# Performance work log

Measured on AMD Instinct MI355X. Metric: run time of the kernel, lower is better.

## Reference

```python
import jax, jax.numpy as jnp
import numpy as np

V, C, H, L, BLK = 32000, 1024, 16, 4, 1024
B, T = 4, 1024
FF = 100
HD = C // H
EPS = 1e-5


def setup_inputs() -> dict:
    key = jax.random.key(0)
    ks = jax.random.split(key, 16)
    n = lambda k, s: (jax.random.normal(k, s, dtype=jnp.float32) * 0.02)
    inp = {
        "idx": jax.random.randint(ks[0], (B, T), 0, V),
        "tok_emb": n(ks[1], (V, C)),
        "pos_emb": n(ks[2], (BLK, C)),
        "Wq": n(ks[3], (L, C, C)), "bq": jnp.zeros((L, C)),
        "Wk": n(ks[4], (L, C, C)), "bk": jnp.zeros((L, C)),
        "Wv": n(ks[5], (L, C, C)), "bv": jnp.zeros((L, C)),
        "Wo": n(ks[6], (L, C, C)), "bo": jnp.zeros((L, C)),
        "ln1_w": jnp.ones((L, C)), "ln1_b": jnp.zeros((L, C)),
        "ln2_w": jnp.ones((L, C)), "ln2_b": jnp.zeros((L, C)),
        "W1": n(ks[7], (L, C, FF)), "b1": jnp.zeros((L, FF)),
        "W2": n(ks[8], (L, FF, C)), "b2": jnp.zeros((L, C)),
        "lnf_w": jnp.ones((C,)), "lnf_b": jnp.zeros((C,)),
    }
    return inp


def _ln(x, w, b):
    m = jnp.mean(x, -1, keepdims=True)
    v = jnp.mean(jnp.square(x - m), -1, keepdims=True)
    return (x - m) * jax.lax.rsqrt(v + EPS) * w + b


def reference(idx, tok_emb, pos_emb, Wq, bq, Wk, bk, Wv, bv, Wo, bo,
              ln1_w, ln1_b, ln2_w, ln2_b, W1, b1, W2, b2, lnf_w, lnf_b):
    Bn, Tn = idx.shape
    x = tok_emb[idx] + pos_emb[:Tn][None]  # [B,T,C]; dropout is identity at eval
    scale = 1.0 / np.sqrt(HD).astype(np.float32)
    att_maps = []
    for l in range(L):
        h = _ln(x, ln1_w[l], ln1_b[l])
        q = (h @ Wq[l] + bq[l]).reshape(Bn, Tn, H, HD).transpose(0, 2, 1, 3)
        k = (h @ Wk[l] + bk[l]).reshape(Bn, Tn, H, HD).transpose(0, 2, 1, 3)
        v = (h @ Wv[l] + bv[l]).reshape(Bn, Tn, H, HD).transpose(0, 2, 1, 3)
        att = jax.nn.softmax(jnp.einsum("bhqd,bhkd->bhqk", q, k) * scale, axis=-1)
        y = jnp.einsum("bhqk,bhkd->bhqd", att, v).transpose(0, 2, 1, 3).reshape(Bn, Tn, C)
        x = x + (y @ Wo[l] + bo[l])
        f = _ln(x, ln2_w[l], ln2_b[l])
        f = jax.nn.relu(f @ W1[l] + b1[l]) @ W2[l] + b2[l]
        x = x + f
        att_maps.append(att.mean(0))  # [H,T,T]
    x = _ln(x, lnf_w, lnf_b)
    pooled = x.mean(1)  # [B,C]
    return pooled, jnp.stack(att_maps)  # [L,H,T,T]
```

## Files before the change

### kernel.cpp

```cpp
#include <hip/hip_runtime.h>

typedef __bf16 bf16;
typedef __bf16 bf16x4 __attribute__((ext_vector_type(4)));
typedef __bf16 bf16x8 __attribute__((ext_vector_type(8)));
typedef float  f32x4  __attribute__((ext_vector_type(4)));

static constexpr int kC   = 1024;
static constexpr int kT   = 1024;
static constexpr int kB   = 4;
static constexpr int kH   = 16;
static constexpr int kHD  = 64;
static constexpr int kL   = 4;
static constexpr int kFF  = 100;
static constexpr int kFFP = 128;
static constexpr int kM   = kB * kT;

__device__ __forceinline__ void gload16(const bf16* g, bf16* l)
{
    __builtin_amdgcn_global_load_lds(
        (const __attribute__((address_space(1))) void*)g,
        (__attribute__((address_space(3))) void*)l, 16, 0, 0);
}

__device__ __forceinline__ unsigned bpack(float a, float b)
{
    bf16 x = (bf16)a, y = (bf16)b;
    unsigned short ux = __builtin_bit_cast(unsigned short, x);
    unsigned short uy = __builtin_bit_cast(unsigned short, y);
    return (unsigned)ux | ((unsigned)uy << 16);
}
__device__ __forceinline__ float blo(unsigned u) { return __builtin_bit_cast(float, u << 16); }
__device__ __forceinline__ float bhi(unsigned u) { return __builtin_bit_cast(float, u & 0xffff0000u); }

__global__ __launch_bounds__(256)
void prep_kernel(const float* __restrict__ Wq, const float* __restrict__ Wk,
                 const float* __restrict__ Wv, const float* __restrict__ Wo,
                 const float* __restrict__ W1, const float* __restrict__ W2,
                 const float* __restrict__ bq, const float* __restrict__ bk,
                 const float* __restrict__ bv,
                 bf16* __restrict__ WQKVT, bf16* __restrict__ WOT,
                 bf16* __restrict__ W1T, bf16* __restrict__ W2T,
                 float* __restrict__ BQKV, float* __restrict__ pooled)
{
    __shared__ float tile[32][33];
    const int bid = blockIdx.x, tid = threadIdx.x;
    const float* src; bf16* dst; int K, N, KP, NP, bx, by;
    if (bid < 12288) {
        const int slab = bid >> 10, within = bid & 1023;
        const int l = slab / 3, which = slab % 3;
        const float* W = (which == 0) ? Wq : (which == 1) ? Wk : Wv;
        src = W + (long)l * kC * kC;
        dst = WQKVT + (long)l * 3 * kC * kC + (long)which * kC * kC;
        K = N = KP = NP = kC; bx = within & 31; by = within >> 5;
    } else if (bid < 16384) {
        const int t = bid - 12288, z = t >> 10, within = t & 1023;
        src = Wo + (long)z * kC * kC; dst = WOT + (long)z * kC * kC;
        K = N = KP = NP = kC; bx = within & 31; by = within >> 5;
    } else if (bid < 16896) {
        const int t = bid - 16384, z = t >> 7, within = t & 127;
        src = W1 + (long)z * kC * kFF; dst = W1T + (long)z * kFFP * kC;
        K = kC; N = kFF; KP = kC; NP = kFFP; bx = within & 3; by = within >> 2;
    } else if (bid < 17408) {
        const int t = bid - 16896, z = t >> 7, within = t & 127;
        src = W2 + (long)z * kFF * kC; dst = W2T + (long)z * kC * kFFP;
        K = kFF; N = kC; KP = kFFP; NP = kC; bx = within & 31; by = within >> 5;
    } else if (bid < 17456) {
        const int gid = (bid - 17408) * 256 + tid;
        const int l = gid / (3 * kC), wq = (gid / kC) % 3, c = gid & (kC - 1);
        const float* s = (wq == 0) ? bq : (wq == 1) ? bk : bv;
        BQKV[gid] = s[l * kC + c];
        return;
    } else {
        const int i = (bid - 17456) * 256 + tid;
        if (i < kB * kC) pooled[i] = 0.f;
        return;
    }
    const int n0 = bx * 32, k0 = by * 32;
    const int tx = tid & 31, ty = tid >> 5;
#pragma unroll
    for (int i = 0; i < 4; ++i) {
        int k = k0 + ty + i * 8, n = n0 + tx;
        tile[ty + i * 8][tx] = (k < K && n < N) ? src[(long)k * N + n] : 0.f;
    }
    __syncthreads();
#pragma unroll
    for (int i = 0; i < 4; ++i) {
        int n = n0 + ty + i * 8, k = k0 + tx;
        if (n < NP && k < KP) dst[(long)n * KP + k] = (bf16)tile[tx][ty + i * 8];
    }
}

__global__ __launch_bounds__(256)
void embed_kernel(const int* __restrict__ idx, const float* __restrict__ tok,
                  const float* __restrict__ pos, float* __restrict__ x)
{
    const int m = blockIdx.x;
    const int c = threadIdx.x * 4;
    const int t = m & (kT - 1);
    const long tk = (long)idx[m] * kC;
    float4 a = *(const float4*)&tok[tk + c];
    float4 b = *(const float4*)&pos[(long)t * kC + c];
    float4 o; o.x = a.x + b.x; o.y = a.y + b.y; o.z = a.z + b.z; o.w = a.w + b.w;
    *(float4*)&x[(long)m * kC + c] = o;
}

__global__ __launch_bounds__(256)
void ln_kernel(const float* __restrict__ x, const float* __restrict__ g,
               const float* __restrict__ be, bf16* __restrict__ ob)
{
    __shared__ float red[8];
    const long row = blockIdx.x;
    const int tid = threadIdx.x, lane = tid & 63, wv = tid >> 6;
    const float4 v = *(const float4*)&x[row * kC + tid * 4];
    float s = v.x + v.y + v.z + v.w;
    float s2 = v.x * v.x + v.y * v.y + v.z * v.z + v.w * v.w;
#pragma unroll
    for (int o = 32; o > 0; o >>= 1) { s += __shfl_down(s, o); s2 += __shfl_down(s2, o); }
    if (!lane) { red[wv] = s; red[4 + wv] = s2; }
    __syncthreads();
    s  = red[0] + red[1] + red[2] + red[3];
    s2 = red[4] + red[5] + red[6] + red[7];
    const float mean = s * (1.f / kC);
    const float var  = s2 * (1.f / kC) - mean * mean;
    const float rstd = rsqrtf(var + 1e-5f);
    const float4 gg = *(const float4*)&g[tid * 4];
    const float4 bb = *(const float4*)&be[tid * 4];
    bf16x4 o;
    o[0] = (bf16)((v.x - mean) * rstd * gg.x + bb.x);
    o[1] = (bf16)((v.y - mean) * rstd * gg.y + bb.y);
    o[2] = (bf16)((v.z - mean) * rstd * gg.z + bb.z);
    o[3] = (bf16)((v.w - mean) * rstd * gg.w + bb.w);
    *(bf16x4*)&ob[row * kC + tid * 4] = o;
}

template<int WAVES_M, int WAVES_N, int AI, int BJ, int MODE, int GL>
__global__ __launch_bounds__(256)
void gemm_bf16(const bf16* __restrict__ Ag, long strideA,
               const bf16* __restrict__ Bg, long strideB,
               const float* __restrict__ bias, int strideBias,
               bf16* __restrict__ outb, long strideOut,
               float* __restrict__ resid,
               int N, int K, int lda, int ldb)
{
    constexpr int BM = WAVES_M * AI * 16;
    constexpr int BN = WAVES_N * BJ * 16;
    constexpr int BK = 64;
    constexpr int LK = GL ? BK : (BK + 8);
    __shared__ __align__(16) bf16 As[BM * LK];
    __shared__ __align__(16) bf16 Bs[BN * LK];
    const int tid = threadIdx.x, lane = tid & 63, wv = tid >> 6;
    const int wm = wv / WAVES_N, wn = wv % WAVES_N;
    const int lr = lane & 15, lg = lane >> 4;
    const int z = blockIdx.z;
    const bf16* A = Ag + (long)z * strideA;
    const bf16* B = Bg + (long)z * strideB;
    const float* bi = bias ? bias + (long)z * strideBias : nullptr;
    const int m0 = blockIdx.y * BM, n0 = blockIdx.x * BN;

    f32x4 acc[AI][BJ];
#pragma unroll
    for (int i = 0; i < AI; ++i)
#pragma unroll
        for (int j = 0; j < BJ; ++j) acc[i][j] = (f32x4){0.f, 0.f, 0.f, 0.f};

    for (int k0 = 0; k0 < K; k0 += BK) {
        if constexpr (GL) {
            static_assert((BM % 32) == 0 && (BN % 32) == 0, "GL tile multiple of 32");
            const int sr  = lane >> 3;
            const int gcb = (lane & 7) ^ sr;
            constexpr int ARW = BM / 4;
            constexpr int BRW = BN / 4;
#pragma unroll
            for (int p = 0; p < BM / 32; ++p)
                gload16(A + (long)(m0 + wv * ARW + p * 8 + sr) * lda + k0 + gcb * 8,
                        &As[(wv * ARW + p * 8) * BK]);
#pragma unroll
            for (int p = 0; p < BN / 32; ++p)
                gload16(B + (long)(n0 + wv * BRW + p * 8 + sr) * ldb + k0 + gcb * 8,
                        &Bs[(wv * BRW + p * 8) * BK]);
        } else {
            constexpr int AP = (BM * BK) / (256 * 8);
#pragma unroll
            for (int p = 0; p < AP; ++p) {
                int r = p * 32 + (tid >> 3), c = (tid & 7) * 8;
                *(uint4*)&As[r * LK + c] = *(const uint4*)&A[(long)(m0 + r) * lda + k0 + c];
            }
            constexpr int BP = (BN * BK) / (256 * 8);
#pragma unroll
            for (int p = 0; p < BP; ++p) {
                int r = p * 32 + (tid >> 3), c = (tid & 7) * 8;
                *(uint4*)&Bs[r * LK + c] = *(const uint4*)&B[(long)(n0 + r) * ldb + k0 + c];
            }
        }
        __syncthreads();
#pragma unroll
        for (int kk = 0; kk < 2; ++kk) {
            bf16x8 af[AI], bfv[BJ];
#pragma unroll
            for (int i = 0; i < AI; ++i) {
                const int r = wm * AI * 16 + i * 16 + lr;
                const int c = GL ? (((kk * 4 + lg) ^ (lr & 7)) * 8) : (kk * 32 + lg * 8);
                af[i] = *(const bf16x8*)&As[r * LK + c];
            }
#pragma unroll
            for (int j = 0; j < BJ; ++j) {
                const int r = wn * BJ * 16 + j * 16 + lr;
                const int c = GL ? (((kk * 4 + lg) ^ (lr & 7)) * 8) : (kk * 32 + lg * 8);
                bfv[j] = *(const bf16x8*)&Bs[r * LK + c];
            }
#pragma unroll
            for (int i = 0; i < AI; ++i)
#pragma unroll
                for (int j = 0; j < BJ; ++j)
                    acc[i][j] = __builtin_amdgcn_mfma_f32_16x16x32_bf16(af[i], bfv[j], acc[i][j], 0, 0, 0);
        }
        __syncthreads();
    }

#pragma unroll
    for (int i = 0; i < AI; ++i)
#pragma unroll
        for (int j = 0; j < BJ; ++j)
#pragma unroll
            for (int rr = 0; rr < 4; ++rr) {
                const int grow = m0 + wm * AI * 16 + i * 16 + lg * 4 + rr;
                const int gcol = n0 + wn * BJ * 16 + j * 16 + lr;
                float v = acc[i][j][rr];
                if constexpr (MODE == 0) {
                    v += bi[gcol];
                    if (z == 0) v *= 0.125f * 1.44269504f;
                    const int b = grow >> 10, t = grow & (kT - 1);
                    const int hh = gcol >> 6, hd = gcol & 63;
                    long o = (long)z * strideOut;
                    if (z == 2) o += (((long)b * kH + hh) * kHD + hd) * kT + t;
                    else        o += (((long)b * kH + hh) * kT + t) * kHD + hd;
                    outb[o] = (bf16)v;
                } else {
                    v += bi[gcol];
                    resid[(long)grow * N + gcol] += v;
                }
            }
}

__global__ __launch_bounds__(256, 2)
void ff_fused(float* __restrict__ X, const float* __restrict__ g,
              const float* __restrict__ be,
              const bf16* __restrict__ W1T_, const float* __restrict__ b1_,
              const bf16* __restrict__ W2T_, const float* __restrict__ b2_)
{
    __shared__ __align__(16) bf16 Hs[16 * kC];
    __shared__ __align__(16) bf16 F1s[16 * kFFP];
    const int tid = threadIdx.x, lane = tid & 63, w = tid >> 6;
    const int lr = lane & 15, lg = lane >> 4;
    const int r0 = blockIdx.x * 16;

    {
        const int row = tid >> 4, c16 = tid & 15;
        float4 xv[16];
        float s1 = 0.f, s2 = 0.f;
#pragma unroll
        for (int p = 0; p < 8; ++p) {
            const float* base = &X[(long)(r0 + row) * kC + p * 128 + c16 * 8];
            xv[2 * p]     = *(const float4*)base;
            xv[2 * p + 1] = *(const float4*)(base + 4);
#pragma unroll
            for (int e = 0; e < 4; ++e) {
                float a0 = ((const float*)&xv[2 * p])[e], a1 = ((const float*)&xv[2 * p + 1])[e];
                s1 += a0 + a1; s2 += a0 * a0 + a1 * a1;
            }
        }
#pragma unroll
        for (int off = 1; off < 16; off <<= 1) { s1 += __shfl_xor(s1, off); s2 += __shfl_xor(s2, off); }
        const float mean = s1 * (1.f / kC);
        const float rstd = rsqrtf(s2 * (1.f / kC) - mean * mean + 1e-5f);
#pragma unroll
        for (int p = 0; p < 8; ++p) {
            const int c0 = p * 128 + c16 * 8;
            float4 g0 = *(const float4*)&g[c0],  g1 = *(const float4*)&g[c0 + 4];
            float4 b0 = *(const float4*)&be[c0], b1v = *(const float4*)&be[c0 + 4];
            float h[8];
#pragma unroll
            for (int e = 0; e < 4; ++e) {
                h[e]     = (((const float*)&xv[2 * p])[e]     - mean) * rstd * ((const float*)&g0)[e] + ((const float*)&b0)[e];
                h[4 + e] = (((const float*)&xv[2 * p + 1])[e] - mean) * rstd * ((const float*)&g1)[e] + ((const float*)&b1v)[e];
            }
            uint4 hv;
            hv.x = bpack(h[0], h[1]); hv.y = bpack(h[2], h[3]);
            hv.z = bpack(h[4], h[5]); hv.w = bpack(h[6], h[7]);
            const int cb = c16 + p * 16;
            *(uint4*)&Hs[row * kC + ((cb ^ (row & 7)) << 3)] = hv;
        }
    }
    __syncthreads();

    {
        f32x4 accA[2], accB[2];
#pragma unroll
        for (int j = 0; j < 2; ++j) { accA[j] = (f32x4){0,0,0,0}; accB[j] = (f32x4){0,0,0,0}; }
        for (int k0 = 0; k0 < kC; k0 += 64) {
            const bf16x8 a0 = *(const bf16x8*)&Hs[lr * kC + ((((k0 >> 3) + 0 * 4 + lg) ^ (lr & 7)) << 3)];
            const bf16x8 a1 = *(const bf16x8*)&Hs[lr * kC + ((((k0 >> 3) + 1 * 4 + lg) ^ (lr & 7)) << 3)];
#pragma unroll
            for (int j = 0; j < 2; ++j) {
                const bf16x8 b0 = *(const bf16x8*)&W1T_[(long)(w * 32 + j * 16 + lr) * kC + k0 + 0 * 32 + lg * 8];
                const bf16x8 b1 = *(const bf16x8*)&W1T_[(long)(w * 32 + j * 16 + lr) * kC + k0 + 1 * 32 + lg * 8];
                accA[j] = __builtin_amdgcn_mfma_f32_16x16x32_bf16(a0, b0, accA[j], 0, 0, 0);
                accB[j] = __builtin_amdgcn_mfma_f32_16x16x32_bf16(a1, b1, accB[j], 0, 0, 0);
            }
        }
#pragma unroll
        for (int j = 0; j < 2; ++j)
#pragma unroll
            for (int rr = 0; rr < 4; ++rr) {
                const int row = lg * 4 + rr, col = w * 32 + j * 16 + lr;
                float v = accA[j][rr] + accB[j][rr] + (col < kFF ? b1_[col] : 0.f);
                F1s[row * kFFP + (((col >> 3) ^ (row & 7)) << 3) + (col & 7)] = (bf16)fmaxf(v, 0.f);
            }
    }
    __syncthreads();

    for (int nc = 0; nc < 8; ++nc) {
        f32x4 acc[2];
        acc[0] = (f32x4){0.f, 0.f, 0.f, 0.f};
        acc[1] = (f32x4){0.f, 0.f, 0.f, 0.f};
#pragma unroll
        for (int kk = 0; kk < 4; ++kk) {
            const bf16x8 a = *(const bf16x8*)&F1s[lr * kFFP + (((kk * 4 + lg) ^ (lr & 7)) << 3)];
#pragma unroll
            for (int j = 0; j < 2; ++j) {
                const bf16x8 bv = *(const bf16x8*)&W2T_[(long)(nc * 128 + w * 32 + j * 16 + lr) * kFFP + kk * 32 + lg * 8];
                acc[j] = __builtin_amdgcn_mfma_f32_16x16x32_bf16(a, bv, acc[j], 0, 0, 0);
            }
        }
#pragma unroll
        for (int j = 0; j < 2; ++j)
#pragma unroll
            for (int rr = 0; rr < 4; ++rr) {
                const int row = r0 + lg * 4 + rr, col = nc * 128 + w * 32 + j * 16 + lr;
                X[(long)row * kC + col] += acc[j][rr] + b2_[col];
            }
    }
}

__global__ __launch_bounds__(256, 2)
void attn_fused(const bf16* __restrict__ Qg, const bf16* __restrict__ Kg,
                const bf16* __restrict__ VTg, bf16* __restrict__ yg,
                float* __restrict__ attm)
{
    __shared__ __align__(16) bf16 SH[32768];
    bf16* Klds = SH;
    bf16* Vlds = SH + 8192;
    bf16* Ps   = SH + 16384;
    __shared__ __align__(16) float reds[16][4];
    __shared__ float invs[16];
    const int tid = threadIdx.x, lane = tid & 63, w = tid >> 6;
    const int lr = lane & 15, lg = lane >> 4;
    const int bid = blockIdx.x, r_ = bid >> 3;
    const int h = ((bid & 7) << 1) | (r_ & 1);
    const int q0 = (r_ >> 1) * 16;

    const int sr  = lane >> 3;
    const int gcb = (lane & 7) ^ sr;
    const int loB = (lg & 1) * 4;
    const int rowb = w * 16 + sr;
    const int ldK0 = (w * 16) * 64, ldK1 = (w * 16 + 8) * 64;

    unsigned am_[16][2];
#pragma unroll
    for (int j = 0; j < 16; ++j) { am_[j][0] = 0u; am_[j][1] = 0u; }

    {
        const bf16* Kb0 = Kg + (long)h * kT * kHD;
        const bf16* Vb0 = VTg + (long)h * kHD * kT;
        gload16(Kb0 + (rowb)     * kHD + gcb * 8, &Klds[ldK0]);
        gload16(Kb0 + (rowb + 8) * kHD + gcb * 8, &Klds[ldK1]);
        gload16(Vb0 + (long)(rowb)     * kT + gcb * 8, &Vlds[ldK0]);
        gload16(Vb0 + (long)(rowb + 8) * kT + gcb * 8, &Vlds[ldK1]);
    }

    for (int b = 0; b < kB; ++b) {
        const long bh = (long)b * kH + h;
        const bf16* Qb = Qg + (bh * kT + q0) * kHD;
        const bf16* Kb = Kg + bh * kT * kHD;
        const bf16* Vb = VTg + bh * (long)kHD * kT;
        const bf16* Kbn = Kg + (bh + kH) * kT * kHD;
        const bf16* Vbn = VTg + (bh + kH) * (long)kHD * kT;

        const bf16x8 qf0 = *(const bf16x8*)&Qb[lr * kHD + lg * 8];
        const bf16x8 qf1 = *(const bf16x8*)&Qb[lr * kHD + 32 + lg * 8];

        float s = 0.f;
        f32x4 y0 = (f32x4){0.f, 0.f, 0.f, 0.f};
        f32x4 y1 = (f32x4){0.f, 0.f, 0.f, 0.f};

#pragma unroll
        for (int kt = 0; kt < 16; ++kt) {
            const int cur = ((b * 16 + kt) & 1) * 4096;
            const int nxt = 4096 - cur;
            if (kt < 15) {
                const int kn = (kt + 1) * 64;
                gload16(Kb + (kn + rowb)     * kHD + gcb * 8, &Klds[nxt + ldK0]);
                gload16(Kb + (kn + rowb + 8) * kHD + gcb * 8, &Klds[nxt + ldK1]);
                gload16(Vb + (long)(rowb)     * kT + kn + gcb * 8, &Vlds[nxt + ldK0]);
                gload16(Vb + (long)(rowb + 8) * kT + kn + gcb * 8, &Vlds[nxt + ldK1]);
            } else if (b < kB - 1) {
                gload16(Kbn + (rowb)     * kHD + gcb * 8, &Klds[nxt + ldK0]);
                gload16(Kbn + (rowb + 8) * kHD + gcb * 8, &Klds[nxt + ldK1]);
                gload16(Vbn + (long)(rowb)     * kT + gcb * 8, &Vlds[nxt + ldK0]);
                gload16(Vbn + (long)(rowb + 8) * kT + gcb * 8, &Vlds[nxt + ldK1]);
            }
            if (kt == 15 && b == kB - 1) {
                asm volatile("s_waitcnt vmcnt(0)" ::: "memory");
            } else {
                asm volatile("s_waitcnt vmcnt(4)" ::: "memory");
            }
            __builtin_amdgcn_sched_barrier(0);

            const int krow = w * 16 + lr;
            const bf16x8 kf0 = *(const bf16x8*)&Klds[cur + krow * 64 + (((0 + lg) ^ (lr & 7)) << 3)];
            const bf16x8 kf1 = *(const bf16x8*)&Klds[cur + krow * 64 + (((4 + lg) ^ (lr & 7)) << 3)];
            f32x4 a = (f32x4){0.f, 0.f, 0.f, 0.f};
            a = __builtin_amdgcn_mfma_f32_16x16x32_bf16(kf0, qf0, a, 0, 0, 0);
            a = __builtin_amdgcn_mfma_f32_16x16x32_bf16(kf1, qf1, a, 0, 0, 0);
            const float e0 = exp2f(a[0]), e1 = exp2f(a[1]);
            const float e2 = exp2f(a[2]), e3 = exp2f(a[3]);
            s += (e0 + e1) + (e2 + e3);
            const int tb = kt * 8 + w * 2 + (lg >> 1);
            uint2 pk; pk.x = bpack(e0, e1); pk.y = bpack(e2, e3);
            *(uint2*)&Ps[lr * kT + ((tb ^ (lr & 7)) << 3) + loB] = pk;

            asm volatile("s_waitcnt lgkmcnt(0)" ::: "memory");
            __builtin_amdgcn_s_barrier();
            __builtin_amdgcn_sched_barrier(0);

            const int vrow = w * 16 + lr;
            const bf16x8 a0 = *(const bf16x8*)&Ps[lr * kT + (((kt * 8 + 0 + lg) ^ (lr & 7)) << 3)];
            const bf16x8 v0 = *(const bf16x8*)&Vlds[cur + vrow * 64 + (((0 + lg) ^ (lr & 7)) << 3)];
            const bf16x8 a1 = *(const bf16x8*)&Ps[lr * kT + (((kt * 8 + 4 + lg) ^ (lr & 7)) << 3)];
            const bf16x8 v1 = *(const bf16x8*)&Vlds[cur + vrow * 64 + (((4 + lg) ^ (lr & 7)) << 3)];
            y0 = __builtin_amdgcn_mfma_f32_16x16x32_bf16(a0, v0, y0, 0, 0, 0);
            y1 = __builtin_amdgcn_mfma_f32_16x16x32_bf16(a1, v1, y1, 0, 0, 0);
        }

        s += __shfl_xor(s, 16);
        s += __shfl_xor(s, 32);
        if (lane < 16) reds[lane][w] = s;
        asm volatile("s_waitcnt lgkmcnt(0)" ::: "memory");
        __builtin_amdgcn_s_barrier();
        __builtin_amdgcn_sched_barrier(0);
        float4 rv = *(const float4*)&reds[lr][0];
        const float inv = __builtin_amdgcn_rcpf((rv.x + rv.y) + (rv.z + rv.w));
        const float iv4 = inv * 0.25f;
        if (lane < 16) invs[lane] = inv;

#pragma unroll
        for (int kt = 0; kt < 16; ++kt) {
            const int tb = kt * 8 + w * 2 + (lg >> 1);
            uint2 e2v = *(const uint2*)&Ps[lr * kT + ((tb ^ (lr & 7)) << 3) + loB];
#pragma unroll
            for (int d = 0; d < 2; ++d) {
                unsigned ev = d ? e2v.y : e2v.x;
                unsigned av = am_[kt][d];
                float n0 = blo(av) + blo(ev) * iv4;
                float n1 = bhi(av) + bhi(ev) * iv4;
                am_[kt][d] = bpack(n0, n1);
            }
        }

#pragma unroll
        for (int rr = 0; rr < 4; ++rr) {
            const float iv = invs[lg * 4 + rr];
            yg[((long)b * kT + q0 + lg * 4 + rr) * kC + h * kHD + w * 16 + lr]
                = (bf16)((y0[rr] + y1[rr]) * iv);
        }
    }

    __syncthreads();
    float* amf = (float*)SH;
#pragma unroll
    for (int kt = 0; kt < 16; ++kt)
#pragma unroll
        for (int d = 0; d < 2; ++d) {
            unsigned av = am_[kt][d];
            const int col = kt * 64 + w * 16 + lg * 4 + 2 * d;
            amf[lr * kT + col]     = blo(av);
            amf[lr * kT + col + 1] = bhi(av);
        }
    __syncthreads();
#pragma unroll
    for (int p = 0; p < 16; ++p) {
        const int f = p * 256 + tid;
        const int row = f >> 8, c4 = f & 255;
        float4 v = *(const float4*)&amf[row * kT + c4 * 4];
        *(float4*)&attm[((long)h * kT + q0 + row) * kT + c4 * 4] = v;
    }
}

__global__ __launch_bounds__(256)
void pool_kernel(const bf16* __restrict__ hb, float* __restrict__ pooled)
{
    const int c = blockIdx.x * 256 + threadIdx.x;
    const int b = blockIdx.y;
    const int t0 = blockIdx.z * 128;
    float s = 0.f;
    for (int t = t0; t < t0 + 128; ++t) s += (float)hb[((long)b * kT + t) * kC + c];
    atomicAdd(&pooled[b * kC + c], s * (1.f / kT));
}

extern "C" void kernel_launch(void* const* d_in, const int* in_sizes, int n_in,
                              void* d_out, int out_size, void* d_ws, size_t ws_size,
                              hipStream_t stream)
{
    const int*   idx  = (const int*)d_in[0];
    const float* tok  = (const float*)d_in[1];
    const float* pos  = (const float*)d_in[2];
    const float* Wq   = (const float*)d_in[3];
    const float* bq   = (const float*)d_in[4];
    const float* Wk   = (const float*)d_in[5];
    const float* bk   = (const float*)d_in[6];
    const float* Wv   = (const float*)d_in[7];
    const float* bv   = (const float*)d_in[8];
    const float* Wo   = (const float*)d_in[9];
    const float* bo   = (const float*)d_in[10];
    const float* ln1w = (const float*)d_in[11];
    const float* ln1b = (const float*)d_in[12];
    const float* ln2w = (const float*)d_in[13];
    const float* ln2b = (const float*)d_in[14];
    const float* W1   = (const float*)d_in[15];
    const float* b1   = (const float*)d_in[16];
    const float* W2   = (const float*)d_in[17];
    const float* b2   = (const float*)d_in[18];
    const float* lnfw = (const float*)d_in[19];
    const float* lnfb = (const float*)d_in[20];

    char* ws = (char*)d_ws;
    long off = 0;
    auto alloc = [&](long bytes) { char* p = ws + off; off += (bytes + 255) & ~255L; return p; };
    bf16*  WQKVT = (bf16*)alloc((long)kL * 3 * kC * kC * 2);
    bf16*  WOT   = (bf16*)alloc((long)kL * kC * kC * 2);
    bf16*  W1T   = (bf16*)alloc((long)kL * kFFP * kC * 2);
    bf16*  W2T   = (bf16*)alloc((long)kL * kC * kFFP * 2);
    float* BQKV  = (float*)alloc((long)kL * 3 * kC * 4);
    float* X     = (float*)alloc((long)kM * kC * 4);
    bf16*  Hbuf  = (bf16*)alloc((long)kM * kC * 2);
    bf16*  QKV   = (bf16*)alloc(3L * kM * kC * 2);
    bf16*  Y     = (bf16*)alloc((long)kM * kC * 2);

    float* pooled = (float*)d_out;
    float* attm_base = pooled + kB * kC;

    prep_kernel<<<17472, 256, 0, stream>>>(Wq, Wk, Wv, Wo, W1, W2, bq, bk, bv,
                                           WQKVT, WOT, W1T, W2T, BQKV, pooled);
    embed_kernel<<<kM, 256, 0, stream>>>(idx, tok, pos, X);

    for (int l = 0; l < kL; ++l) {
        ln_kernel<<<kM, 256, 0, stream>>>(X, ln1w + l * kC, ln1b + l * kC, Hbuf);
        gemm_bf16<2, 2, 4, 4, 0, 1><<<dim3(8, 32, 3), 256, 0, stream>>>(
            Hbuf, 0L, WQKVT + (long)l * 3 * kC * kC, (long)kC * kC,
            BQKV + l * 3 * kC, kC, QKV, (long)kM * kC, nullptr,
            kC, kC, kC, kC);
        attn_fused<<<dim3(1024), 256, 0, stream>>>(
            QKV, QKV + (long)kM * kC, QKV + 2L * kM * kC, Y,
            attm_base + (long)l * kH * kT * kT);
        gemm_bf16<2, 2, 4, 4, 4, 1><<<dim3(8, 32, 1), 256, 0, stream>>>(
            Y, 0L, WOT + (long)l * kC * kC, 0L, bo + l * kC, 0,
            nullptr, 0L, X, kC, kC, kC, kC);
        ff_fused<<<256, 256, 0, stream>>>(X, ln2w + l * kC, ln2b + l * kC,
                                          W1T + (long)l * kFFP * kC, b1 + l * kFF,
                                          W2T + (long)l * kC * kFFP, b2 + l * kC);
    }
    ln_kernel<<<kM, 256, 0, stream>>>(X, lnfw, lnfb, Hbuf);
    pool_kernel<<<dim3(4, kB, 8), 256, 0, stream>>>(Hbuf, pooled);
}
```

Baseline: 900.2 us.

## Replace direct global-to-LDS K/V prefetch with register-staged two-tile-ahead pipeline

The attention kernel stops using global_load_lds with vmcnt waits to double-buffer K/V tiles. It now loads K/V tiles into registers two tiles ahead and writes them to LDS after the P store, before the existing barrier. The goal is to hide global-load latency more deeply and avoid explicit vmcnt stalls. The cost is more VGPRs, extra LDS write instructions, and a non-overlapped initial load at the start of each batch.

```diff
diff --git a/kernel.cpp b/kernel.cpp
--- a/kernel.cpp
+++ b/kernel.cpp
@@ -364,30 +364,33 @@
     const int loB = (lg & 1) * 4;
     const int rowb = w * 16 + sr;
     const int ldK0 = (w * 16) * 64, ldK1 = (w * 16 + 8) * 64;
+    const int wr8 = lane * 8;
 
     unsigned am_[16][2];
 #pragma unroll
     for (int j = 0; j < 16; ++j) { am_[j][0] = 0u; am_[j][1] = 0u; }
-
-    {
-        const bf16* Kb0 = Kg + (long)h * kT * kHD;
-        const bf16* Vb0 = VTg + (long)h * kHD * kT;
-        gload16(Kb0 + (rowb)     * kHD + gcb * 8, &Klds[ldK0]);
-        gload16(Kb0 + (rowb + 8) * kHD + gcb * 8, &Klds[ldK1]);
-        gload16(Vb0 + (long)(rowb)     * kT + gcb * 8, &Vlds[ldK0]);
-        gload16(Vb0 + (long)(rowb + 8) * kT + gcb * 8, &Vlds[ldK1]);
-    }
 
     for (int b = 0; b < kB; ++b) {
         const long bh = (long)b * kH + h;
         const bf16* Qb = Qg + (bh * kT + q0) * kHD;
         const bf16* Kb = Kg + bh * kT * kHD;
         const bf16* Vb = VTg + bh * (long)kHD * kT;
-        const bf16* Kbn = Kg + (bh + kH) * kT * kHD;
-        const bf16* Vbn = VTg + (bh + kH) * (long)kHD * kT;
 
         const bf16x8 qf0 = *(const bf16x8*)&Qb[lr * kHD + lg * 8];
         const bf16x8 qf1 = *(const bf16x8*)&Qb[lr * kHD + 32 + lg * 8];
+
+        uint4 kA0 = *(const uint4*)(Kb + (rowb)     * kHD + gcb * 8);
+        uint4 kA1 = *(const uint4*)(Kb + (rowb + 8) * kHD + gcb * 8);
+        uint4 vA0 = *(const uint4*)(Vb + (long)(rowb)     * kT + gcb * 8);
+        uint4 vA1 = *(const uint4*)(Vb + (long)(rowb + 8) * kT + gcb * 8);
+        uint4 kB0 = *(const uint4*)(Kb + (64 + rowb)     * kHD + gcb * 8);
+        uint4 kB1 = *(const uint4*)(Kb + (64 + rowb + 8) * kHD + gcb * 8);
+        uint4 vB0 = *(const uint4*)(Vb + (long)(rowb)     * kT + 64 + gcb * 8);
+        uint4 vB1 = *(const uint4*)(Vb + (long)(rowb + 8) * kT + 64 + gcb * 8);
+        *(uint4*)&Klds[ldK0 + wr8] = kA0;
+        *(uint4*)&Klds[ldK1 + wr8] = kA1;
+        *(uint4*)&Vlds[ldK0 + wr8] = vA0;
+        *(uint4*)&Vlds[ldK1 + wr8] = vA1;
 
         float s = 0.f;
         f32x4 y0 = (f32x4){0.f, 0.f, 0.f, 0.f};
@@ -395,26 +398,22 @@
 
 #pragma unroll
         for (int kt = 0; kt < 16; ++kt) {
-            const int cur = ((b * 16 + kt) & 1) * 4096;
+            const int cur = (kt & 1) * 4096;
             const int nxt = 4096 - cur;
-            if (kt < 15) {
-                const int kn = (kt + 1) * 64;
-                gload16(Kb + (kn + rowb)     * kHD + gcb * 8, &Klds[nxt + ldK0]);
-                gload16(Kb + (kn + rowb + 8) * kHD + gcb * 8, &Klds[nxt + ldK1]);
-                gload16(Vb + (long)(rowb)     * kT + kn + gcb * 8, &Vlds[nxt + ldK0]);
-                gload16(Vb + (long)(rowb + 8) * kT + kn + gcb * 8, &Vlds[nxt + ldK1]);
-            } else if (b < kB - 1) {
-                gload16(Kbn + (rowb)     * kHD + gcb * 8, &Klds[nxt + ldK0]);
-                gload16(Kbn + (rowb + 8) * kHD + gcb * 8, &Klds[nxt + ldK1]);
-                gload16(Vbn + (long)(rowb)     * kT + gcb * 8, &Vlds[nxt + ldK0]);
-                gload16(Vbn + (long)(rowb + 8) * kT + gcb * 8, &Vlds[nxt + ldK1]);
-            }
-            if (kt == 15 && b == kB - 1) {
-                asm volatile("s_waitcnt vmcnt(0)" ::: "memory");
-            } else {
-                asm volatile("s_waitcnt vmcnt(4)" ::: "memory");
-            }
-            __builtin_amdgcn_sched_barrier(0);
+            if (kt < 14) {
+                const int kn = (kt + 2) * 64;
+                if ((kt & 1) == 0) {
+                    kA0 = *(const uint4*)(Kb + (kn + rowb)     * kHD + gcb * 8);
+                    kA1 = *(const uint4*)(Kb + (kn + rowb + 8) * kHD + gcb * 8);
+                    vA0 = *(const uint4*)(Vb + (long)(rowb)     * kT + kn + gcb * 8);
+                    vA1 = *(const uint4*)(Vb + (long)(rowb + 8) * kT + kn + gcb * 8);
+                } else {
+                    kB0 = *(const uint4*)(Kb + (kn + rowb)     * kHD + gcb * 8);
+                    kB1 = *(const uint4*)(Kb + (kn + rowb + 8) * kHD + gcb * 8);
+                    vB0 = *(const uint4*)(Vb + (long)(rowb)     * kT + kn + gcb * 8);
+                    vB1 = *(const uint4*)(Vb + (long)(rowb + 8) * kT + kn + gcb * 8);
+                }
+            }
 
             const int krow = w * 16 + lr;
             const bf16x8 kf0 = *(const bf16x8*)&Klds[cur + krow * 64 + (((0 + lg) ^ (lr & 7)) << 3)];
@@ -428,6 +427,20 @@
             const int tb = kt * 8 + w * 2 + (lg >> 1);
             uint2 pk; pk.x = bpack(e0, e1); pk.y = bpack(e2, e3);
             *(uint2*)&Ps[lr * kT + ((tb ^ (lr & 7)) << 3) + loB] = pk;
+
+            if (kt < 15) {
+                if ((kt & 1) == 0) {
+                    *(uint4*)&Klds[nxt + ldK0 + wr8] = kB0;
+                    *(uint4*)&Klds[nxt + ldK1 + wr8] = kB1;
+                    *(uint4*)&Vlds[nxt + ldK0 + wr8] = vB0;
+                    *(uint4*)&Vlds[nxt + ldK1 + wr8] = vB1;
+                } else {
+                    *(uint4*)&Klds[nxt + ldK0 + wr8] = kA0;
+                    *(uint4*)&Klds[nxt + ldK1 + wr8] = kA1;
+                    *(uint4*)&Vlds[nxt + ldK0 + wr8] = vA0;
+                    *(uint4*)&Vlds[nxt + ldK1 + wr8] = vA1;
+                }
+            }
 
             asm volatile("s_waitcnt lgkmcnt(0)" ::: "memory");
             __builtin_amdgcn_s_barrier();
```

Result: faster. 817.7 us (median of 2 runs) (-9.2%).
